# Kernel tuning notes

Hardware: AMD Instinct MI355X
Metric: run time of the kernel (lower is better)

The kernel has to match this reference:

```python
import jax, jax.numpy as jnp
import numpy as np

L = 12          # layers
H = 12          # heads
D = 768         # hidden
HD = 64         # head dim
FF = 3072       # ffn dim
VOCAB = 50265
MAXPOS = 2050
WINDOWS = (32, 32, 64, 64, 128, 128, 256, 256, 512, 512, 512, 512)
EPS = 1e-5


def layer_norm(x, g, b):
    mu = jnp.mean(x, axis=-1, keepdims=True)
    var = jnp.mean(jnp.square(x - mu), axis=-1, keepdims=True)
    return (x - mu) * jax.lax.rsqrt(var + EPS) * g + b


def sliding_window_attention(q, k, v, key_add, half):
    """Banded (Longformer local) attention.
    q,k,v: [B,H,S,hd]; key_add: [B,S] additive mask; window one-sided = half.
    Queries are chunked into blocks of `half`; each block's band lies inside a
    3*half key span, so we never materialize an SxS matrix."""
    B, nh, S, hd = q.shape
    nc = S // half
    w3 = 3 * half
    qc = q.reshape(B, nh, nc, half, hd) * (1.0 / jnp.sqrt(jnp.asarray(hd, q.dtype)))
    kp = jnp.pad(k, ((0, 0), (0, 0), (half, half), (0, 0)))
    vp = jnp.pad(v, ((0, 0), (0, 0), (half, half), (0, 0)))
    ap = jnp.pad(key_add, ((0, 0), (half, half)))
    idx = jnp.arange(nc)[:, None] * half + jnp.arange(w3)[None, :]  # [nc, 3h]
    kc = kp[:, :, idx]   # [B,H,nc,3h,hd]
    vc = vp[:, :, idx]
    ac = ap[:, idx]      # [B,nc,3h]
    scores = jnp.einsum('bhcqd,bhckd->bhcqk', qc, kc)
    scores = scores + ac[:, None, :, None, :]
    qpos = jnp.arange(half)[:, None]
    kpos = jnp.arange(w3)[None, :]
    band = (kpos >= qpos) & (kpos <= qpos + 2 * half)            # [half,3h]
    gk = jnp.arange(nc)[:, None] * half - half + jnp.arange(w3)[None, :]
    valid = (gk >= 0) & (gk < S)                                  # [nc,3h]
    m = band[None, :, :] & valid[:, None, :]                      # [nc,half,3h]
    scores = jnp.where(m[None, None], scores, -1e9)
    p = jax.nn.softmax(scores, axis=-1)
    out = jnp.einsum('bhcqk,bhckd->bhcqd', p, vc)
    return out.reshape(B, nh, S, hd)


def setup_inputs() -> dict:
    key = jax.random.key(0)
    ks = jax.random.split(key, 32)
    B, S = 2, 2048
    s = 0.02
    inp = {
        'ids': jax.random.randint(ks[0], (B, S), 0, VOCAB),
        'mask': jnp.ones((B, S), jnp.float32),
        'fts': jax.random.normal(ks[1], (B, 1), jnp.float32),
        'word_emb': jax.random.normal(ks[2], (VOCAB, D)) * s,
        'pos_emb': jax.random.normal(ks[3], (MAXPOS, D)) * s,
        'type_emb': jax.random.normal(ks[4], (1, D)) * s,
        'ln_emb_g': jnp.ones((D,)), 'ln_emb_b': jnp.zeros((D,)),
        'Wq': jax.random.normal(ks[5], (L, D, D)) * s, 'bq': jnp.zeros((L, D)),
        'Wk': jax.random.normal(ks[6], (L, D, D)) * s, 'bk': jnp.zeros((L, D)),
        'Wv': jax.random.normal(ks[7], (L, D, D)) * s, 'bv': jnp.zeros((L, D)),
        'Wo': jax.random.normal(ks[8], (L, D, D)) * s, 'bo': jnp.zeros((L, D)),
        'ln1_g': jnp.ones((L, D)), 'ln1_b': jnp.zeros((L, D)),
        'W1': jax.random.normal(ks[9], (L, D, FF)) * s, 'b1': jnp.zeros((L, FF)),
        'W2': jax.random.normal(ks[10], (L, FF, D)) * s, 'b2': jnp.zeros((L, D)),
        'ln2_g': jnp.ones((L, D)), 'ln2_b': jnp.zeros((L, D)),
        'Wtop': jax.random.normal(ks[11], (D + 1, 1)) * s, 'btop': jnp.zeros((1,)),
    }
    return inp


def reference(ids, mask, fts, word_emb, pos_emb, type_emb, ln_emb_g, ln_emb_b,
              Wq, bq, Wk, bk, Wv, bv, Wo, bo, ln1_g, ln1_b,
              W1, b1, W2, b2, ln2_g, ln2_b, Wtop, btop):
    B, S = ids.shape
    # RoBERTa-style positions with padding_idx=1 (mask assumed all-valid)
    pos = jnp.arange(S) + 2
    x = word_emb[ids] + pos_emb[pos][None] + type_emb[0][None, None]
    x = layer_norm(x, ln_emb_g, ln_emb_b)
    key_add = (1.0 - mask) * -1e9  # additive key padding mask [B,S]
    for i in range(L):
        half = WINDOWS[i] // 2
        q = (x @ Wq[i] + bq[i]).reshape(B, S, H, HD).transpose(0, 2, 1, 3)
        k = (x @ Wk[i] + bk[i]).reshape(B, S, H, HD).transpose(0, 2, 1, 3)
        v = (x @ Wv[i] + bv[i]).reshape(B, S, H, HD).transpose(0, 2, 1, 3)
        a = sliding_window_attention(q, k, v, key_add, half)
        a = a.transpose(0, 2, 1, 3).reshape(B, S, D)
        x = layer_norm(x + a @ Wo[i] + bo[i], ln1_g[i], ln1_b[i])
        h = jax.nn.gelu(x @ W1[i] + b1[i], approximate=False)
        x = layer_norm(x + h @ W2[i] + b2[i], ln2_g[i], ln2_b[i])
    cls = x[:, 0, :]
    out = jnp.concatenate([cls, fts], axis=1) @ Wtop + btop
    return out
```

## Files before the change

kernel.cpp:

```cpp
#include <hip/hip_runtime.h>

typedef unsigned short u16;
using short8   = __attribute__((ext_vector_type(8))) short;
using floatx4  = __attribute__((ext_vector_type(4))) float;
using ushortx4 = __attribute__((ext_vector_type(4))) unsigned short;

static const int g_halves[12] = {16,16,32,32,64,64,128,128,256,256,256,256};

__device__ __forceinline__ float bf2f(u16 u) {
  union { unsigned int i; float f; } x; x.i = ((unsigned int)u) << 16; return x.f;
}
__device__ __forceinline__ u16 f2bf(float f) {
  union { float f; unsigned int i; } x; x.f = f;
  unsigned int r = x.i + 0x7FFFu + ((x.i >> 16) & 1u);
  return (u16)(r >> 16);
}

__device__ __forceinline__ void gld_lds16(const u16* g, u16* l) {
  __builtin_amdgcn_global_load_lds(
      (const __attribute__((address_space(1))) unsigned int*)g,
      (__attribute__((address_space(3))) unsigned int*)l, 16, 0, 0);
}

__global__ __launch_bounds__(256) void transpose_cvt(
    const float* __restrict__ in, u16* __restrict__ out, int R, int C,
    size_t inZ, size_t outZ)
{
  __shared__ u16 t[32][33];
  const int tx = threadIdx.x & 31, ty = threadIdx.x >> 5;
  const size_t bi = (size_t)blockIdx.z * inZ;
  const size_t bo = (size_t)blockIdx.z * outZ;
  const int r0 = blockIdx.y * 32, c0 = blockIdx.x * 32;
#pragma unroll
  for (int j = 0; j < 32; j += 8)
    t[ty + j][tx] = f2bf(in[bi + (size_t)(r0 + ty + j) * C + (c0 + tx)]);
  __syncthreads();
#pragma unroll
  for (int j = 0; j < 32; j += 8)
    out[bo + (size_t)(c0 + ty + j) * R + (r0 + tx)] = t[tx][ty + j];
}

template<int EPI>
__global__ __launch_bounds__(256) void gemm_bt(
    const u16* __restrict__ A, const u16* __restrict__ Bt,
    const float* __restrict__ biasA, const float* __restrict__ biasB, const float* __restrict__ biasC,
    float* __restrict__ outF, u16* __restrict__ outB,
    u16* __restrict__ qg, u16* __restrict__ kg, u16* __restrict__ vt,
    int M, int N, int K, int KC)
{
  __shared__ __align__(16) u16 lsA[128 * 32];
  __shared__ __align__(16) u16 lsB[128 * 32];
  const int tid  = threadIdx.x;
  const int wave = tid >> 6, lane = tid & 63;
  const int quad = lane >> 4, l16 = lane & 15;
  const int m0 = blockIdx.y * 128, n0 = blockIdx.x * 128;
  const int kz = blockIdx.z * KC;
  const int wm = (wave >> 1) * 64, wn = (wave & 1) * 64;
  const int srow = lane >> 2;
  const int skof = (lane & 3) * 8;

  floatx4 acc[4][4] = {};

  for (int k0 = kz; k0 < kz + KC; k0 += 32) {
    __syncthreads();
#pragma unroll
    for (int c = wave; c < 16; c += 4) {
      if (c < 8)
        gld_lds16(A  + (size_t)(m0 + c * 16 + srow) * K + k0 + skof, lsA + c * 512);
      else
        gld_lds16(Bt + (size_t)(n0 + (c - 8) * 16 + srow) * K + k0 + skof, lsB + (c - 8) * 512);
    }
    __syncthreads();
    short8 af[4], bfr[4];
#pragma unroll
    for (int i = 0; i < 4; ++i)
      af[i]  = *(const short8*)(lsA + (wm + i * 16 + l16) * 32 + quad * 8);
#pragma unroll
    for (int j = 0; j < 4; ++j)
      bfr[j] = *(const short8*)(lsB + (wn + j * 16 + l16) * 32 + quad * 8);
#pragma unroll
    for (int i = 0; i < 4; ++i)
#pragma unroll
      for (int j = 0; j < 4; ++j)
        acc[i][j] = __builtin_amdgcn_mfma_f32_16x16x32_bf16(af[i], bfr[j], acc[i][j], 0, 0, 0);
  }

#pragma unroll
  for (int i = 0; i < 4; ++i)
#pragma unroll
    for (int j = 0; j < 4; ++j) {
      const int col = n0 + wn + j * 16 + l16;
      if (EPI == 3) {
        const int seg = (col >= 1536) ? 2 : (col >= 768) ? 1 : 0;
        const int cc = col - seg * 768;
        const int hh = cc >> 6, dd = cc & 63;
        const float bvl = (seg == 0) ? biasA[cc] : (seg == 1) ? biasB[cc] : biasC[cc];
        const int row0 = m0 + wm + i * 16 + quad * 4;
        const int bI = row0 >> 11, ss = row0 & 2047;
        const int bh = bI * 12 + hh;
        if (seg == 2) {
          ushortx4 pk;
#pragma unroll
          for (int r = 0; r < 4; ++r) pk[r] = f2bf(acc[i][j][r] + bvl);
          *(ushortx4*)(vt + ((size_t)bh * 64 + dd) * 2048 + ss) = pk;
        } else {
          u16* dst = (seg == 0) ? qg : kg;
          const float scl = (seg == 0) ? 0.125f : 1.0f;
#pragma unroll
          for (int r = 0; r < 4; ++r)
            dst[((size_t)bh * 2048 + ss + r) * 64 + dd] = f2bf((acc[i][j][r] + bvl) * scl);
        }
      } else if (EPI == 2) {
        const float bvl = biasA[col];
#pragma unroll
        for (int r = 0; r < 4; ++r) {
          const int row = m0 + wm + i * 16 + quad * 4 + r;
          const size_t idx = (size_t)row * N + col;
          float v = acc[i][j][r] + bvl;
          v = 0.5f * v * (1.0f + erff(v * 0.70710678118654752f));
          outB[idx] = f2bf(v);
        }
      } else {
#pragma unroll
        for (int r = 0; r < 4; ++r) {
          const int row = m0 + wm + i * 16 + quad * 4 + r;
          outF[((size_t)blockIdx.z * M + row) * N + col] = acc[i][j][r];
        }
      }
    }
}

__global__ __launch_bounds__(256) void attn_mfma(
    const u16* __restrict__ q_g, const u16* __restrict__ k_g,
    const u16* __restrict__ vt_g, const float* __restrict__ mask,
    u16* __restrict__ ab, int halfw)
{
  __shared__ __align__(16) u16 lsP[4][640];

  const int b = blockIdx.z, h = blockIdx.y;
  const int bh = b * 12 + h;
  const int wave = threadIdx.x >> 6, lane = threadIdx.x & 63;
  const int quad = lane >> 4, l16 = lane & 15;
  const int qw0 = blockIdx.x * 64 + wave * 16;

  const size_t qrow = ((size_t)bh * 2048 + qw0 + l16) * 64 + quad * 8;
  const short8 qf0 = *(const short8*)(q_g + qrow);
  const short8 qf1 = *(const short8*)(q_g + qrow + 32);

  floatx4 oacc[4] = {};
  float lrow[4] = {0.f, 0.f, 0.f, 0.f};
  u16* Pw = lsP[wave];

  const int klo = ((qw0 - halfw > 0) ? (qw0 - halfw) : 0) & ~31;
  const int khi = (qw0 + 15 + halfw < 2047) ? (qw0 + 15 + halfw) : 2047;

  for (int k0 = klo; k0 <= khi; k0 += 32) {
    floatx4 sc[2];
#pragma unroll
    for (int ct = 0; ct < 2; ++ct) {
      const size_t kr = ((size_t)bh * 2048 + k0 + ct * 16 + l16) * 64 + quad * 8;
      const short8 kf0 = *(const short8*)(k_g + kr);
      const short8 kf1 = *(const short8*)(k_g + kr + 32);
      floatx4 sa = {};
      sa = __builtin_amdgcn_mfma_f32_16x16x32_bf16(qf0, kf0, sa, 0, 0, 0);
      sa = __builtin_amdgcn_mfma_f32_16x16x32_bf16(qf1, kf1, sa, 0, 0, 0);
      sc[ct] = sa;
    }
    float pr[2][4];
#pragma unroll
    for (int ct = 0; ct < 2; ++ct) {
      const int g = k0 + ct * 16 + l16;
      const int gc = (g < 2047) ? g : 2047;
      const float ma = (1.0f - mask[b * 2048 + gc]) * -1.0e9f;
#pragma unroll
      for (int r = 0; r < 4; ++r) {
        const int t = qw0 + quad * 4 + r;
        const bool valid = (g >= t - halfw) && (g <= t + halfw) && (g < 2048);
        pr[ct][r] = __expf(valid ? sc[ct][r] + ma : -1.0e9f);
      }
    }
#pragma unroll
    for (int r = 0; r < 4; ++r) {
      float rs = pr[0][r] + pr[1][r];
      rs += __shfl_xor(rs, 1, 64);
      rs += __shfl_xor(rs, 2, 64);
      rs += __shfl_xor(rs, 4, 64);
      rs += __shfl_xor(rs, 8, 64);
      lrow[r] += rs;
    }
#pragma unroll
    for (int ct = 0; ct < 2; ++ct)
#pragma unroll
      for (int r = 0; r < 4; ++r)
        Pw[(quad * 4 + r) * 40 + ct * 16 + l16] = f2bf(pr[ct][r]);
    const short8 pa = *(const short8*)(Pw + l16 * 40 + quad * 8);
#pragma unroll
    for (int dt = 0; dt < 4; ++dt) {
      const size_t vr = ((size_t)bh * 64 + dt * 16 + l16) * 2048 + k0 + quad * 8;
      const short8 vf = *(const short8*)(vt_g + vr);
      oacc[dt] = __builtin_amdgcn_mfma_f32_16x16x32_bf16(pa, vf, oacc[dt], 0, 0, 0);
    }
  }

#pragma unroll
  for (int r = 0; r < 4; ++r) {
    const float inv = 1.0f / lrow[r];
    const size_t orow = ((size_t)b * 2048 + qw0 + quad * 4 + r) * 768 + h * 64;
#pragma unroll
    for (int dt = 0; dt < 4; ++dt)
      ab[orow + dt * 16 + l16] = f2bf(oacc[dt][r] * inv);
  }
}

__global__ __launch_bounds__(256) void embed_ln_kernel(
    const int* __restrict__ ids, const float* __restrict__ wemb, const float* __restrict__ pemb,
    const float* __restrict__ temb, const float* __restrict__ g, const float* __restrict__ be,
    float* __restrict__ x, u16* __restrict__ xb)
{
  const int t = blockIdx.x;
  const int s = t & 2047;
  const int id = ids[t];
  const int tid = threadIdx.x;
  const int wave = tid >> 6, lane = tid & 63;

  float vals[3]; float sum = 0.f, ssq = 0.f;
#pragma unroll
  for (int i = 0; i < 3; ++i) {
    const int d = tid + i * 256;
    const float v = wemb[(size_t)id * 768 + d] + pemb[(size_t)(s + 2) * 768 + d] + temb[d];
    vals[i] = v; sum += v; ssq += v * v;
  }
#pragma unroll
  for (int off = 32; off; off >>= 1) { sum += __shfl_xor(sum, off, 64); ssq += __shfl_xor(ssq, off, 64); }
  __shared__ float rb[8];
  if (lane == 0) { rb[wave] = sum; rb[4 + wave] = ssq; }
  __syncthreads();
  sum = rb[0] + rb[1] + rb[2] + rb[3];
  ssq = rb[4] + rb[5] + rb[6] + rb[7];
  const float mu = sum * (1.f / 768.f);
  const float var = ssq * (1.f / 768.f) - mu * mu;
  const float rstd = rsqrtf(var + 1e-5f);
#pragma unroll
  for (int i = 0; i < 3; ++i) {
    const int d = tid + i * 256;
    const float o = (vals[i] - mu) * rstd * g[d] + be[d];
    x[(size_t)t * 768 + d] = o;
    xb[(size_t)t * 768 + d] = f2bf(o);
  }
}

template<int NC>
__global__ __launch_bounds__(256) void reduce_ln_kernel(
    const float* __restrict__ pb, const float* __restrict__ bias,
    const float* __restrict__ g, const float* __restrict__ be,
    float* x, u16* __restrict__ xb)
{
  const int t = blockIdx.x;
  const int tid = threadIdx.x;
  const int wave = tid >> 6, lane = tid & 63;

  float vals[3]; float sum = 0.f, ssq = 0.f;
#pragma unroll
  for (int i = 0; i < 3; ++i) {
    const int d = tid + i * 256;
    float v = x[(size_t)t * 768 + d] + bias[d];
#pragma unroll
    for (int c = 0; c < NC; ++c)
      v += pb[((size_t)c * 4096 + t) * 768 + d];
    vals[i] = v; sum += v; ssq += v * v;
  }
#pragma unroll
  for (int off = 32; off; off >>= 1) { sum += __shfl_xor(sum, off, 64); ssq += __shfl_xor(ssq, off, 64); }
  __shared__ float rb[8];
  if (lane == 0) { rb[wave] = sum; rb[4 + wave] = ssq; }
  __syncthreads();
  sum = rb[0] + rb[1] + rb[2] + rb[3];
  ssq = rb[4] + rb[5] + rb[6] + rb[7];
  const float mu = sum * (1.f / 768.f);
  const float var = ssq * (1.f / 768.f) - mu * mu;
  const float rstd = rsqrtf(var + 1e-5f);
#pragma unroll
  for (int i = 0; i < 3; ++i) {
    const int d = tid + i * 256;
    const float o = (vals[i] - mu) * rstd * g[d] + be[d];
    x[(size_t)t * 768 + d] = o;
    xb[(size_t)t * 768 + d] = f2bf(o);
  }
}

__global__ __launch_bounds__(256) void head_kernel(
    const float* __restrict__ x, const float* __restrict__ fts,
    const float* __restrict__ wtop, const float* __restrict__ btop, float* __restrict__ out)
{
  const int tid = threadIdx.x;
  const int wave = tid >> 6, lane = tid & 63;
  __shared__ float rb[4];
  for (int b = 0; b < 2; ++b) {
    float s = 0.f;
    for (int d = tid; d < 768; d += 256)
      s += x[(size_t)b * 2048 * 768 + d] * wtop[d];
#pragma unroll
    for (int off = 32; off; off >>= 1) s += __shfl_xor(s, off, 64);
    if (lane == 0) rb[wave] = s;
    __syncthreads();
    if (tid == 0) {
      float r = rb[0] + rb[1] + rb[2] + rb[3];
      r += fts[b] * wtop[768] + btop[0];
      out[b] = r;
    }
    __syncthreads();
  }
}

extern "C" void kernel_launch(void* const* d_in, const int* in_sizes, int n_in,
                              void* d_out, int out_size, void* d_ws, size_t ws_size,
                              hipStream_t stream)
{
  const int*   ids  = (const int*)d_in[0];
  const float* mask = (const float*)d_in[1];
  const float* fts  = (const float*)d_in[2];
  const float* wemb = (const float*)d_in[3];
  const float* pemb = (const float*)d_in[4];
  const float* temb = (const float*)d_in[5];
  const float* lneg = (const float*)d_in[6];
  const float* lneb = (const float*)d_in[7];
  const float* Wq   = (const float*)d_in[8];
  const float* bq   = (const float*)d_in[9];
  const float* Wk   = (const float*)d_in[10];
  const float* bk   = (const float*)d_in[11];
  const float* Wv   = (const float*)d_in[12];
  const float* bvv  = (const float*)d_in[13];
  const float* Wo   = (const float*)d_in[14];
  const float* bo   = (const float*)d_in[15];
  const float* ln1g = (const float*)d_in[16];
  const float* ln1b = (const float*)d_in[17];
  const float* W1   = (const float*)d_in[18];
  const float* b1   = (const float*)d_in[19];
  const float* W2   = (const float*)d_in[20];
  const float* b2   = (const float*)d_in[21];
  const float* ln2g = (const float*)d_in[22];
  const float* ln2b = (const float*)d_in[23];
  const float* wtop = (const float*)d_in[24];
  const float* btop = (const float*)d_in[25];

  const size_t SQ   = 768 * 768;
  const size_t SQ3  = 2304 * 768;
  const size_t SF   = 3072 * 768;
  const size_t perL = SQ3 + SQ + 2 * SF;
  const size_t NTOK = 4096;
  const size_t HDSZ = (size_t)2 * 12 * 2048 * 64;
  const size_t PAD  = 4096;

  const size_t fixedBytes =
      NTOK * 768 * 4
    + NTOK * 768 * 2
    + 4 * NTOK * 768 * 4
    + NTOK * 768 * 2
    + NTOK * 3072 * 2
    + 3 * (HDSZ + PAD) * 2;
  const bool batched = ws_size >= fixedBytes + 12 * perL * 2 + 65536;
  const size_t nw = batched ? 12 : 1;

  char* p = (char*)d_ws;
  u16* wTqkv = (u16*)p; p += nw * SQ3 * 2;
  u16* wTo   = (u16*)p; p += nw * SQ  * 2;
  u16* wT1   = (u16*)p; p += nw * SF  * 2;
  u16* wT2   = (u16*)p; p += nw * SF  * 2;
  float* x  = (float*)p; p += NTOK * 768 * 4;
  u16*   xb = (u16*)p;   p += NTOK * 768 * 2;
  float* pb = (float*)p; p += 4 * NTOK * 768 * 4;
  u16*   ab = (u16*)p;   p += NTOK * 768 * 2;
  u16*   hb = (u16*)p;   p += NTOK * 3072 * 2;
  u16*   qB  = (u16*)p;  p += (HDSZ + PAD) * 2;
  u16*   kB  = (u16*)p;  p += (HDSZ + PAD) * 2;
  u16*   vtB = (u16*)p;  p += (HDSZ + PAD) * 2;

  if (batched) {
    transpose_cvt<<<dim3(24, 24, 12), 256, 0, stream>>>(Wq, wTqkv,             768, 768,  SQ, SQ3);
    transpose_cvt<<<dim3(24, 24, 12), 256, 0, stream>>>(Wk, wTqkv + 768 * 768, 768, 768,  SQ, SQ3);
    transpose_cvt<<<dim3(24, 24, 12), 256, 0, stream>>>(Wv, wTqkv + 1536 * 768,768, 768,  SQ, SQ3);
    transpose_cvt<<<dim3(24, 24, 12), 256, 0, stream>>>(Wo, wTo, 768, 768,  SQ, SQ);
    transpose_cvt<<<dim3(96, 24, 12), 256, 0, stream>>>(W1, wT1, 768, 3072, SF, SF);
    transpose_cvt<<<dim3(24, 96, 12), 256, 0, stream>>>(W2, wT2, 3072, 768, SF, SF);
  }

  embed_ln_kernel<<<4096, 256, 0, stream>>>(ids, wemb, pemb, temb, lneg, lneb, x, xb);

  for (int i = 0; i < 12; ++i) {
    const u16 *WqkvTl, *WoTl, *W1Tl, *W2Tl;
    if (batched) {
      WqkvTl = wTqkv + (size_t)i * SQ3; WoTl = wTo + (size_t)i * SQ;
      W1Tl = wT1 + (size_t)i * SF;      W2Tl = wT2 + (size_t)i * SF;
    } else {
      transpose_cvt<<<dim3(24, 24, 1), 256, 0, stream>>>(Wq + (size_t)i * SQ, wTqkv,             768, 768, SQ, SQ3);
      transpose_cvt<<<dim3(24, 24, 1), 256, 0, stream>>>(Wk + (size_t)i * SQ, wTqkv + 768 * 768, 768, 768, SQ, SQ3);
      transpose_cvt<<<dim3(24, 24, 1), 256, 0, stream>>>(Wv + (size_t)i * SQ, wTqkv + 1536 * 768,768, 768, SQ, SQ3);
      transpose_cvt<<<dim3(24, 24, 1), 256, 0, stream>>>(Wo + (size_t)i * SQ, wTo, 768, 768, SQ, SQ);
      transpose_cvt<<<dim3(96, 24, 1), 256, 0, stream>>>(W1 + (size_t)i * SF, wT1, 768, 3072, SF, SF);
      transpose_cvt<<<dim3(24, 96, 1), 256, 0, stream>>>(W2 + (size_t)i * SF, wT2, 3072, 768, SF, SF);
      WqkvTl = wTqkv; WoTl = wTo; W1Tl = wT1; W2Tl = wT2;
    }

    gemm_bt<3><<<dim3(18, 32), 256, 0, stream>>>(
        xb, WqkvTl, bq + (size_t)i * 768, bk + (size_t)i * 768, bvv + (size_t)i * 768,
        nullptr, nullptr, qB, kB, vtB, 4096, 2304, 768, 768);

    attn_mfma<<<dim3(32, 12, 2), 256, 0, stream>>>(qB, kB, vtB, mask, ab, g_halves[i]);

    gemm_bt<4><<<dim3(6, 32, 2), 256, 0, stream>>>(
        ab, WoTl, nullptr, nullptr, nullptr, pb, nullptr,
        nullptr, nullptr, nullptr, 4096, 768, 768, 384);
    reduce_ln_kernel<2><<<4096, 256, 0, stream>>>(
        pb, bo + (size_t)i * 768, ln1g + (size_t)i * 768, ln1b + (size_t)i * 768, x, xb);

    gemm_bt<2><<<dim3(24, 32), 256, 0, stream>>>(
        xb, W1Tl, b1 + (size_t)i * 3072, nullptr, nullptr, nullptr, hb,
        nullptr, nullptr, nullptr, 4096, 3072, 768, 768);

    gemm_bt<4><<<dim3(6, 32, 4), 256, 0, stream>>>(
        hb, W2Tl, nullptr, nullptr, nullptr, pb, nullptr,
        nullptr, nullptr, nullptr, 4096, 768, 3072, 768);
    reduce_ln_kernel<4><<<4096, 256, 0, stream>>>(
        pb, b2 + (size_t)i * 768, ln2g + (size_t)i * 768, ln2b + (size_t)i * 768, x, xb);
  }

  head_kernel<<<1, 256, 0, stream>>>(x, fts, wtop, btop, (float*)d_out);
}
```

Baseline: 2.595 ms.

## Add 256x256 eight-wave pipelined GEMM for FFN matmuls

Introduces a new 512-thread GEMM kernel with 256x256 output tiles, double-buffered LDS staged through direct global-to-LDS loads, XOR-swizzled LDS layout, and an interleaved load/MFMA schedule with barriers and raised wave priority during MFMA. The FFN up-projection (with GELU epilogue) and the split-K down-projection now use it instead of the older 128-tile GEMM. The larger tiles raise data reuse per LDS load and the staged prefetch overlaps memory with compute. In exchange, register pressure and LDS use are high (128KB LDS per block), and the grids shrink (192 blocks for both), which may underfill the GPU's compute units.

```diff
diff --git a/kernel.cpp b/kernel.cpp
--- a/kernel.cpp
+++ b/kernel.cpp
@@ -126,6 +126,139 @@
           const int row = m0 + wm + i * 16 + quad * 4 + r;
           outF[((size_t)blockIdx.z * M + row) * N + col] = acc[i][j][r];
         }
+      }
+    }
+}
+
+template<int EPI>
+__global__ __launch_bounds__(512, 2) void gemm8p(
+    const u16* __restrict__ A, const u16* __restrict__ Bt,
+    const float* __restrict__ bias,
+    float* __restrict__ outF, u16* __restrict__ outB,
+    int M, int N, int K, int KC)
+{
+  __shared__ __align__(16) u16 ls[2][2][2][8192];
+  const int tid  = threadIdx.x;
+  const int wave = tid >> 6, lane = tid & 63;
+  const int quad = lane >> 4, l16 = lane & 15;
+  const int lr   = l16 & 7;
+  const int m0 = blockIdx.y * 256, n0 = blockIdx.x * 256;
+  const int kz = blockIdx.z * KC;
+  const int NT = KC >> 6;
+
+  const int ha  = wave >> 2;
+  const int hbw = (wave >> 1) & 1;
+  const int cb  = (wave & 1) * 64;
+  const int wm  = (wave >> 2) * 128;
+  const int wn  = (wave & 3) * 64;
+
+  int srow[2], soff[2];
+#pragma unroll
+  for (int ii = 0; ii < 2; ++ii) {
+    const int g = (ii * 8 + wave) * 64 + lane;
+    srow[ii] = g >> 3;
+    soff[ii] = ((g & 7) ^ (srow[ii] & 7)) * 8;
+  }
+  int cs[2];
+#pragma unroll
+  for (int ks = 0; ks < 2; ++ks) cs[ks] = (((ks << 2) | quad) ^ lr) * 8;
+
+  floatx4 acc[8][4] = {};
+  short8 af[4][2];
+  short8 bf[4][2];
+
+#define STG(buf, op, half, base, rb, kc) do { \
+  _Pragma("unroll") \
+  for (int ii = 0; ii < 2; ++ii) \
+    gld_lds16((base) + (size_t)((rb) + (half) * 128 + srow[ii]) * K + (kc) + soff[ii], \
+              &ls[buf][op][half][(ii * 8 + wave) * 512]); \
+} while (0)
+
+#define RDA(ig) do { \
+  _Pragma("unroll") \
+  for (int ii = 0; ii < 4; ++ii) \
+  _Pragma("unroll") \
+  for (int ks = 0; ks < 2; ++ks) \
+    af[ii][ks] = *(const short8*)&ls[cur][0][ha][(((ig) * 4 + ii) * 16 + l16) * 64 + cs[ks]]; \
+} while (0)
+
+#define RDB(jg) do { \
+  _Pragma("unroll") \
+  for (int jj = 0; jj < 2; ++jj) \
+  _Pragma("unroll") \
+  for (int ks = 0; ks < 2; ++ks) \
+    bf[(jg) * 2 + jj][ks] = *(const short8*)&ls[cur][1][hbw][(cb + ((jg) * 2 + jj) * 16 + l16) * 64 + cs[ks]]; \
+} while (0)
+
+#define MM(ILO, JLO) do { \
+  __builtin_amdgcn_s_setprio(1); \
+  _Pragma("unroll") \
+  for (int ii = 0; ii < 4; ++ii) \
+  _Pragma("unroll") \
+  for (int jj = 0; jj < 2; ++jj) \
+  _Pragma("unroll") \
+  for (int ks = 0; ks < 2; ++ks) \
+    acc[(ILO) + ii][(JLO) + jj] = __builtin_amdgcn_mfma_f32_16x16x32_bf16( \
+        af[ii][ks], bf[(JLO) + jj][ks], acc[(ILO) + ii][(JLO) + jj], 0, 0, 0); \
+  __builtin_amdgcn_s_setprio(0); \
+} while (0)
+
+  STG(0, 1, 0, Bt, n0, kz); STG(0, 1, 1, Bt, n0, kz);
+  STG(0, 0, 0, A,  m0, kz); STG(0, 0, 1, A,  m0, kz);
+  STG(1, 1, 0, Bt, n0, kz + 64); STG(1, 1, 1, Bt, n0, kz + 64);
+  asm volatile("s_waitcnt vmcnt(4)" ::: "memory");
+  __builtin_amdgcn_s_barrier();
+
+  int cur = 0;
+  for (int t = 0; t < NT; ++t, cur ^= 1) {
+    const int k1 = kz + (t + 1) * 64;
+    const int k2 = k1 + 64;
+    const bool s1 = (t + 1 < NT), s2 = (t + 2 < NT);
+    RDA(0); RDB(0);
+    if (s1) STG(cur ^ 1, 0, 0, A, m0, k1);
+    __builtin_amdgcn_s_barrier();
+    MM(0, 0);
+    __builtin_amdgcn_s_barrier();
+    RDB(1);
+    if (s1) STG(cur ^ 1, 0, 1, A, m0, k1);
+    __builtin_amdgcn_s_barrier();
+    MM(0, 2);
+    __builtin_amdgcn_s_barrier();
+    RDA(1);
+    if (s2) STG(cur, 1, 0, Bt, n0, k2);
+    __builtin_amdgcn_s_barrier();
+    MM(4, 2);
+    __builtin_amdgcn_s_barrier();
+    if (s2) STG(cur, 1, 1, Bt, n0, k2);
+    __builtin_amdgcn_s_barrier();
+    MM(4, 0);
+    if (s2) asm volatile("s_waitcnt vmcnt(4)" ::: "memory");
+    else    asm volatile("s_waitcnt vmcnt(0)" ::: "memory");
+    __builtin_amdgcn_s_barrier();
+  }
+#undef STG
+#undef RDA
+#undef RDB
+#undef MM
+
+#pragma unroll
+  for (int i = 0; i < 8; ++i)
+#pragma unroll
+    for (int j = 0; j < 4; ++j) {
+      const int col  = n0 + wn + j * 16 + l16;
+      const int row0 = m0 + wm + i * 16 + quad * 4;
+      if (EPI == 2) {
+        const float bvl = bias[col];
+#pragma unroll
+        for (int r = 0; r < 4; ++r) {
+          float v = acc[i][j][r] + bvl;
+          v = 0.5f * v * (1.0f + erff(v * 0.70710678118654752f));
+          outB[(size_t)(row0 + r) * N + col] = f2bf(v);
+        }
+      } else {
+#pragma unroll
+        for (int r = 0; r < 4; ++r)
+          outF[((size_t)blockIdx.z * M + row0 + r) * N + col] = acc[i][j][r];
       }
     }
 }
@@ -413,13 +546,11 @@
     reduce_ln_kernel<2><<<4096, 256, 0, stream>>>(
         pb, bo + (size_t)i * 768, ln1g + (size_t)i * 768, ln1b + (size_t)i * 768, x, xb);
 
-    gemm_bt<2><<<dim3(24, 32), 256, 0, stream>>>(
-        xb, W1Tl, b1 + (size_t)i * 3072, nullptr, nullptr, nullptr, hb,
-        nullptr, nullptr, nullptr, 4096, 3072, 768, 768);
-
-    gemm_bt<4><<<dim3(6, 32, 4), 256, 0, stream>>>(
-        hb, W2Tl, nullptr, nullptr, nullptr, pb, nullptr,
-        nullptr, nullptr, nullptr, 4096, 768, 3072, 768);
+    gemm8p<2><<<dim3(12, 16), 512, 0, stream>>>(
+        xb, W1Tl, b1 + (size_t)i * 3072, nullptr, hb, 4096, 3072, 768, 768);
+
+    gemm8p<4><<<dim3(3, 16, 4), 512, 0, stream>>>(
+        hb, W2Tl, nullptr, pb, nullptr, 4096, 768, 3072, 768);
     reduce_ln_kernel<4><<<4096, 256, 0, stream>>>(
         pb, b2 + (size_t)i * 768, ln2g + (size_t)i * 768, ln2b + (size_t)i * 768, x, xb);
   }
```

Result: slower. 2.940 ms (+13.3%).
